# Optimization experiments

Hardware: AMD Instinct MI355X
Metric: run time of the kernel (lower is better)

Reference implementation:

```python
import jax, jax.numpy as jnp
import numpy as np

NUM_GRAPHS = 32
NODES_PER_GRAPH = 256
N = NUM_GRAPHS * NODES_PER_GRAPH
IN_CH, HID, OUT_CH = 64, 256, 32
K = 20
SPACE, PROP = 3, 2
NEG_SLOPE = 0.01  # F.leaky_relu default
BIG = 1e9         # cross-graph distance mask


def _glorot(key, shape):
    fan_in, fan_out = shape
    lim = (6.0 / (fan_in + fan_out)) ** 0.5
    return jax.random.uniform(key, shape, jnp.float32, -lim, lim)


def setup_inputs() -> dict:
    key = jax.random.key(0)
    ks = jax.random.split(key, 16)
    inp = {
        "x": jax.random.normal(ks[0], (N, IN_CH), jnp.float32),
        "batch": jnp.repeat(jnp.arange(NUM_GRAPHS, dtype=jnp.int32), NODES_PER_GRAPH),
    }
    dims = [(IN_CH, HID), (HID, HID), (HID, OUT_CH)]
    i = 1
    for li, (cin, cout) in enumerate(dims, start=1):
        inp[f"Ws{li}"] = _glorot(ks[i], (cin, SPACE)); i += 1
        inp[f"bs{li}"] = jnp.zeros((SPACE,), jnp.float32)
        inp[f"Wh{li}"] = _glorot(ks[i], (cin, PROP)); i += 1
        inp[f"bh{li}"] = jnp.zeros((PROP,), jnp.float32)
        inp[f"Wo{li}"] = _glorot(ks[i], (cin + PROP, cout)); i += 1
        inp[f"bo{li}"] = jnp.zeros((cout,), jnp.float32)
    return inp


def gravnet_conv(x, mask_add, Ws, bs, Wh, bh, Wo, bo):
    s = x @ Ws + bs                                     # [N,3] learned coords
    h = x @ Wh + bh                                     # [N,2] propagate feats
    s2 = jnp.sum(s * s, axis=1)
    d2 = s2[:, None] + s2[None, :] - 2.0 * (s @ s.T)    # [N,N] squared dists
    d2 = jnp.maximum(d2, 0.0) + mask_add                # block within-graph only
    neg_d2, idx = jax.lax.top_k(-d2, K)                 # kNN (includes self)
    w = jnp.exp(10.0 * neg_d2)                          # exp(-10 * d^2)
    agg = jnp.einsum('nk,nkp->np', w, h[idx])           # aggr='add'
    return jnp.concatenate([agg, x], axis=-1) @ Wo + bo  # lin(cat([out, x]))


def _leaky(h):
    return jnp.where(h >= 0, h, NEG_SLOPE * h)


def reference(x, batch,
              Ws1, bs1, Wh1, bh1, Wo1, bo1,
              Ws2, bs2, Wh2, bh2, Wo2, bo2,
              Ws3, bs3, Wh3, bh3, Wo3, bo3):
    mask_add = jnp.where(batch[:, None] == batch[None, :], 0.0, BIG).astype(x.dtype)
    # dropout p=0.0 -> identity
    h = _leaky(gravnet_conv(x, mask_add, Ws1, bs1, Wh1, bh1, Wo1, bo1))
    h = _leaky(gravnet_conv(h, mask_add, Ws2, bs2, Wh2, bh2, Wo2, bo2))
    out = gravnet_conv(h, mask_add, Ws3, bs3, Wh3, bh3, Wo3, bo3)
    # get_zero_nodes: first node of each contiguous graph segment
    b = jnp.concatenate([jnp.zeros((1,), batch.dtype), batch])
    diff = (b[1:] - b[:-1]).at[0].set(1)
    first_idx = jnp.nonzero(diff != 0, size=NUM_GRAPHS)[0]
    return out[first_idx]
```

## Files before the change

kernel.cpp:

```cpp
#include <hip/hip_runtime.h>
#include <hip/hip_bf16.h>


#define NGRAPH 32
#define GN 256
#define NTOT (NGRAPH*GN)
#define KNN 20
#define CTS 129

typedef __attribute__((ext_vector_type(8))) short bf16x8;
typedef __attribute__((ext_vector_type(4))) float f32x4;

__device__ __forceinline__ ushort f2bf(float x) {
    union { float f; unsigned u; } a; a.f = x;
    unsigned r = a.u + 0x7FFFu + ((a.u >> 16) & 1u);
    return (ushort)(r >> 16);
}
__device__ __forceinline__ float bf2f(ushort h) {
    union { unsigned u; float f; } b; b.u = ((unsigned)h) << 16;
    return b.f;
}
__device__ __forceinline__ bf16x8 ld8(const ushort* p) {
    return *reinterpret_cast<const bf16x8*>(p);
}
__device__ __forceinline__ unsigned pack2(ushort a, ushort b) {
    return (unsigned)a | ((unsigned)b << 16);
}

__global__ __launch_bounds__(256) void k_front(
    const float* __restrict__ X,
    const float* __restrict__ Ws1, const float* __restrict__ bs1,
    const float* __restrict__ Wh1, const float* __restrict__ bh1,
    const float* __restrict__ Wo1, const float* __restrict__ Wo2,
    const float* __restrict__ bs2, const float* __restrict__ bh2,
    const float* __restrict__ bs3, const float* __restrict__ bh3,
    ushort* __restrict__ Wt1hi, ushort* __restrict__ Wt1lo,
    ushort* __restrict__ Wt2hi, ushort* __restrict__ Wt2lo,
    ushort* __restrict__ Xhi, ushort* __restrict__ Xlo,
    float* __restrict__ s1, float* __restrict__ h1p,
    float* __restrict__ s2, float* __restrict__ h2p,
    float* __restrict__ s3, float* __restrict__ h3p)
{
    int b = blockIdx.x, tid = threadIdx.x;
    if (b < 2048) {
        int gw = b * 4 + (tid >> 6);
        int lane = tid & 63;
        float xv = X[(size_t)gw * 64 + lane];
        float a0 = xv * Ws1[lane * 3 + 0];
        float a1 = xv * Ws1[lane * 3 + 1];
        float a2 = xv * Ws1[lane * 3 + 2];
        float a3 = xv * Wh1[lane * 2 + 0];
        float a4 = xv * Wh1[lane * 2 + 1];
#pragma unroll
        for (int m = 1; m < 64; m <<= 1) {
            a0 += __shfl_xor(a0, m); a1 += __shfl_xor(a1, m); a2 += __shfl_xor(a2, m);
            a3 += __shfl_xor(a3, m); a4 += __shfl_xor(a4, m);
        }
        if (lane == 0) {
            s1[gw * 3 + 0] = a0 + bs1[0];
            s1[gw * 3 + 1] = a1 + bs1[1];
            s1[gw * 3 + 2] = a2 + bs1[2];
            h1p[gw * 2 + 0] = a3 + bh1[0];
            h1p[gw * 2 + 1] = a4 + bh1[1];
        }
    } else if (b < 2368) {
        int t = (b - 2048) * 256 + tid;
        if (t < 65536) {
            int n = t >> 8, c = t & 255;
            float v = Wo2[(size_t)(2 + c) * 256 + n];
            ushort hi = f2bf(v);
            Wt2hi[n * 256 + c] = hi;
            Wt2lo[n * 256 + c] = f2bf(v - bf2f(hi));
        } else {
            int u = t - 65536;
            int n = u >> 6, c = u & 63;
            float v = Wo1[(size_t)(2 + c) * 256 + n];
            ushort hi = f2bf(v);
            Wt1hi[n * 64 + c] = hi;
            Wt1lo[n * 64 + c] = f2bf(v - bf2f(hi));
        }
    } else if (b < 2688) {
        int u = (b - 2368) * 256 + tid;
        if (u < 24576)      s2[u] = bs2[u % 3];
        else if (u < 40960) { int w = u - 24576; h2p[w] = bh2[w & 1]; }
        else if (u < 65536) { int w = u - 40960; s3[w] = bs3[w % 3]; }
        else                { int w = u - 65536; h3p[w] = bh3[w & 1]; }
    } else {
        int t = (b - 2688) * 256 + tid;
        float2 v = *reinterpret_cast<const float2*>(&X[(size_t)t * 2]);
        ushort hx = f2bf(v.x), hy = f2bf(v.y);
        Xhi[t * 2 + 0] = hx; Xlo[t * 2 + 0] = f2bf(v.x - bf2f(hx));
        Xhi[t * 2 + 1] = hy; Xlo[t * 2 + 1] = f2bf(v.y - bf2f(hy));
    }
}

__device__ __forceinline__ void knn_row_agg(
    const float* __restrict__ s, const float* __restrict__ h,
    int base, int row, int lane, float& out0, float& out1)
{
    float s0 = s[row * 3 + 0], s1 = s[row * 3 + 1], s2 = s[row * 3 + 2];
    float s2row = s0 * s0 + s1 * s1 + s2 * s2;
    auto calc = [&](int j) {
        const float* sj = s + (size_t)(base + j) * 3;
        float t0 = sj[0], t1 = sj[1], t2 = sj[2];
        float s2j = t0 * t0 + t1 * t1 + t2 * t2;
        float dot = s0 * t0 + s1 * t1 + s2 * t2;
        float d2 = s2row + s2j - 2.0f * dot;
        return __float_as_uint(d2 > 0.f ? d2 : 0.f);
    };
    unsigned ua = calc(lane),       ub = calc(lane + 64);
    unsigned uc = calc(lane + 128), ud = calc(lane + 192);
    float2 hA = *reinterpret_cast<const float2*>(&h[(size_t)(base + lane) * 2]);
    float2 hB = *reinterpret_cast<const float2*>(&h[(size_t)(base + lane + 64) * 2]);
    float2 hC = *reinterpret_cast<const float2*>(&h[(size_t)(base + lane + 128) * 2]);
    float2 hD = *reinterpret_cast<const float2*>(&h[(size_t)(base + lane + 192) * 2]);

    float acc0 = 0.f, acc1 = 0.f;
#pragma unroll 1
    for (int it = 0; it < KNN; ++it) {
        unsigned bv = ua; float bh0 = hA.x, bh1 = hA.y;
        if (ub < bv) { bv = ub; bh0 = hB.x; bh1 = hB.y; }
        if (uc < bv) { bv = uc; bh0 = hC.x; bh1 = hC.y; }
        if (ud < bv) { bv = ud; bh0 = hD.x; bh1 = hD.y; }
        unsigned gv = bv;
#pragma unroll
        for (int m = 1; m < 64; m <<= 1) {
            unsigned o = __shfl_xor(gv, m);
            gv = o < gv ? o : gv;
        }
        float d2 = __uint_as_float(gv);
        if (d2 > 2.0f) break;
        unsigned long long mask = __ballot(bv == gv);
        int wl = __ffsll(mask) - 1;
        if (lane == wl) {
            float w = __expf(-10.0f * d2);
            acc0 = fmaf(w, bh0, acc0);
            acc1 = fmaf(w, bh1, acc1);
            ua = (ua == gv) ? 0xFFFFFFFFu : ua;
            ub = (ub == gv) ? 0xFFFFFFFFu : ub;
            uc = (uc == gv) ? 0xFFFFFFFFu : uc;
            ud = (ud == gv) ? 0xFFFFFFFFu : ud;
        }
    }
#pragma unroll
    for (int m = 1; m < 64; m <<= 1) {
        acc0 += __shfl_xor(acc0, m);
        acc1 += __shfl_xor(acc1, m);
    }
    out0 = acc0; out1 = acc1;
}

__global__ __launch_bounds__(256) void knn_kernel(
    const float* __restrict__ s, const float* __restrict__ h,
    float* __restrict__ agg)
{
    int gw = (int)(blockIdx.x * 4 + (threadIdx.x >> 6));
    int lane = threadIdx.x & 63;
    float a0, a1;
    knn_row_agg(s, h, gw & ~(GN - 1), gw, lane, a0, a1);
    if (lane == 0) {
        agg[gw * 2 + 0] = a0;
        agg[gw * 2 + 1] = a1;
    }
}

template<int K, int CMODE>
__global__ __launch_bounds__(512) void gemm_fused(
    const ushort* __restrict__ Ahi, const ushort* __restrict__ Alo,
    const ushort* __restrict__ Bhi, const ushort* __restrict__ Blo,
    const float* __restrict__ Wfull, const float* __restrict__ bias,
    const float* __restrict__ agg,
    float* __restrict__ Cf, ushort* __restrict__ Chi, ushort* __restrict__ Clo,
    const float* __restrict__ Wsn, const float* __restrict__ Whn,
    float* __restrict__ s_out, float* __restrict__ h_out)
{
    __shared__ float CT[64 * CTS];
    __shared__ float part[64 * 8 * 5];

    const int tid = threadIdx.x;
    const int lane = tid & 63, wid = tid >> 6;
    const int wm = wid >> 2, wn = wid & 3;
    const int m0 = blockIdx.x * 64, n0 = blockIdx.y * 128;

    f32x4 acc[2][2];
#pragma unroll
    for (int mi = 0; mi < 2; ++mi)
#pragma unroll
        for (int ni = 0; ni < 2; ++ni)
            acc[mi][ni] = (f32x4){0.f, 0.f, 0.f, 0.f};

#pragma unroll 2
    for (int kof = 0; kof < K; kof += 32) {
        int kch = kof + (lane >> 4) * 8;
        bf16x8 ah[2], al[2], bh[2], bl[2];
#pragma unroll
        for (int mi = 0; mi < 2; ++mi) {
            size_t off = (size_t)(m0 + wm * 32 + mi * 16 + (lane & 15)) * K + kch;
            ah[mi] = ld8(Ahi + off); al[mi] = ld8(Alo + off);
        }
#pragma unroll
        for (int ni = 0; ni < 2; ++ni) {
            size_t off = (size_t)(n0 + wn * 32 + ni * 16 + (lane & 15)) * K + kch;
            bh[ni] = ld8(Bhi + off); bl[ni] = ld8(Blo + off);
        }
#pragma unroll
        for (int mi = 0; mi < 2; ++mi)
#pragma unroll
            for (int ni = 0; ni < 2; ++ni) {
                acc[mi][ni] = __builtin_amdgcn_mfma_f32_16x16x32_bf16(ah[mi], bh[ni], acc[mi][ni], 0, 0, 0);
                acc[mi][ni] = __builtin_amdgcn_mfma_f32_16x16x32_bf16(ah[mi], bl[ni], acc[mi][ni], 0, 0, 0);
                acc[mi][ni] = __builtin_amdgcn_mfma_f32_16x16x32_bf16(al[mi], bh[ni], acc[mi][ni], 0, 0, 0);
            }
    }

#pragma unroll
    for (int ni = 0; ni < 2; ++ni) {
        int nl = wn * 32 + ni * 16 + (lane & 15);
        int n = n0 + nl;
        float w0 = Wfull[n], w1 = Wfull[256 + n], bz = bias[n];
#pragma unroll
        for (int mi = 0; mi < 2; ++mi) {
            int mb = wm * 32 + mi * 16 + ((lane >> 4) << 2);
#pragma unroll
            for (int r = 0; r < 4; ++r) {
                int ml = mb + r, m = m0 + ml;
                float v = acc[mi][ni][r] + fmaf(agg[m * 2 + 0], w0, fmaf(agg[m * 2 + 1], w1, bz));
                v = v >= 0.f ? v : 0.01f * v;
                CT[ml * CTS + nl] = v;
                if (CMODE == 1 && (m & 255) == 0) Cf[(m >> 8) * 256 + n] = v;
            }
        }
    }
    __syncthreads();

    if (CMODE == 0) {
        int row = tid >> 3, cbase = (tid & 7) * 16;
        size_t m = (size_t)(m0 + row);
#pragma unroll
        for (int j = 0; j < 2; ++j) {
            int c = cbase + j * 8;
            ushort hi[8], lo[8];
#pragma unroll
            for (int t = 0; t < 8; ++t) {
                float v = CT[row * CTS + c + t];
                hi[t] = f2bf(v);
                lo[t] = f2bf(v - bf2f(hi[t]));
            }
            uint4 wh = make_uint4(pack2(hi[0], hi[1]), pack2(hi[2], hi[3]),
                                  pack2(hi[4], hi[5]), pack2(hi[6], hi[7]));
            uint4 wl = make_uint4(pack2(lo[0], lo[1]), pack2(lo[2], lo[3]),
                                  pack2(lo[4], lo[5]), pack2(lo[6], lo[7]));
            *reinterpret_cast<uint4*>(&Chi[m * 256 + n0 + c]) = wh;
            *reinterpret_cast<uint4*>(&Clo[m * 256 + n0 + c]) = wl;
        }
    }

    {
        int row = tid & 63, sub = tid >> 6;
        float p0 = 0.f, p1 = 0.f, p2 = 0.f, p3 = 0.f, p4 = 0.f;
#pragma unroll
        for (int i = 0; i < 16; ++i) {
            int c = sub * 16 + i;
            float v = CT[row * CTS + c];
            int n = n0 + c;
            p0 = fmaf(v, Wsn[n * 3 + 0], p0);
            p1 = fmaf(v, Wsn[n * 3 + 1], p1);
            p2 = fmaf(v, Wsn[n * 3 + 2], p2);
            p3 = fmaf(v, Whn[n * 2 + 0], p3);
            p4 = fmaf(v, Whn[n * 2 + 1], p4);
        }
        float* pp = &part[(row * 8 + sub) * 5];
        pp[0] = p0; pp[1] = p1; pp[2] = p2; pp[3] = p3; pp[4] = p4;
    }
    __syncthreads();
    if (tid < 320) {
        int row = tid / 5, o = tid - row * 5;
        float sum = 0.f;
#pragma unroll
        for (int k = 0; k < 8; ++k) sum += part[(row * 8 + k) * 5 + o];
        if (o < 3) atomicAdd(&s_out[(m0 + row) * 3 + o], sum);
        else       atomicAdd(&h_out[(m0 + row) * 2 + (o - 3)], sum);
    }
}

__global__ __launch_bounds__(256) void knn3_final(
    const float* __restrict__ s, const float* __restrict__ h,
    const float* __restrict__ h2c,
    const float* __restrict__ Wo, const float* __restrict__ bo,
    float* __restrict__ out)
{
    __shared__ float aggL[2];
    __shared__ float pm[8][32];
    int g = blockIdx.x, tid = threadIdx.x;
    if (tid < 64) {
        float a0, a1;
        knn_row_agg(s, h, g * GN, g * GN, tid, a0, a1);
        if (tid == 0) { aggL[0] = a0; aggL[1] = a1; }
    }
    __syncthreads();
    int o = tid & 31, seg = tid >> 5;
    const float* xr = h2c + g * 256;
    float p = 0.f;
#pragma unroll
    for (int i = 0; i < 32; ++i) {
        int c = seg * 32 + i;
        p = fmaf(xr[c], Wo[(2 + c) * 32 + o], p);
    }
    pm[seg][o] = p;
    __syncthreads();
    if (tid < 32) {
        float acc = fmaf(aggL[0], Wo[o], fmaf(aggL[1], Wo[32 + o], bo[o]));
#pragma unroll
        for (int k = 0; k < 8; ++k) acc += pm[k][o];
        out[g * 32 + o] = acc;
    }
}

extern "C" void kernel_launch(void* const* d_in, const int* in_sizes, int n_in,
                              void* d_out, int out_size, void* d_ws, size_t ws_size,
                              hipStream_t stream) {
    const float* X   = (const float*)d_in[0];
    const float* Ws1 = (const float*)d_in[2];  const float* bs1 = (const float*)d_in[3];
    const float* Wh1 = (const float*)d_in[4];  const float* bh1 = (const float*)d_in[5];
    const float* Wo1 = (const float*)d_in[6];  const float* bo1 = (const float*)d_in[7];
    const float* Ws2 = (const float*)d_in[8];  const float* bs2 = (const float*)d_in[9];
    const float* Wh2 = (const float*)d_in[10]; const float* bh2 = (const float*)d_in[11];
    const float* Wo2 = (const float*)d_in[12]; const float* bo2 = (const float*)d_in[13];
    const float* Ws3 = (const float*)d_in[14]; const float* bs3 = (const float*)d_in[15];
    const float* Wh3 = (const float*)d_in[16]; const float* bh3 = (const float*)d_in[17];
    const float* Wo3 = (const float*)d_in[18]; const float* bo3 = (const float*)d_in[19];

    float* p = (float*)d_ws;
    float* s1   = p; p += NTOT * 3;
    float* hp1  = p; p += NTOT * 2;
    float* s2   = p; p += NTOT * 3;
    float* hp2  = p; p += NTOT * 2;
    float* s3   = p; p += NTOT * 3;
    float* hp3  = p; p += NTOT * 2;
    float* aggb = p; p += NTOT * 2;
    float* h2c  = p; p += 32 * 256;
    ushort* q = (ushort*)p;
    ushort* Xhi  = q; q += (size_t)NTOT * 64;
    ushort* Xlo  = q; q += (size_t)NTOT * 64;
    ushort* h1hi = q; q += (size_t)NTOT * 256;
    ushort* h1lo = q; q += (size_t)NTOT * 256;
    ushort* Wt1hi = q; q += 256 * 64;
    ushort* Wt1lo = q; q += 256 * 64;
    ushort* Wt2hi = q; q += 256 * 256;
    ushort* Wt2lo = q; q += 256 * 256;

    k_front<<<3712, 256, 0, stream>>>(X, Ws1, bs1, Wh1, bh1, Wo1, Wo2,
                                      bs2, bh2, bs3, bh3,
                                      Wt1hi, Wt1lo, Wt2hi, Wt2lo, Xhi, Xlo,
                                      s1, hp1, s2, hp2, s3, hp3);
    knn_kernel<<<2048, 256, 0, stream>>>(s1, hp1, aggb);
    gemm_fused<64, 0><<<dim3(128, 2), 512, 0, stream>>>(Xhi, Xlo, Wt1hi, Wt1lo,
                                                        Wo1, bo1, aggb,
                                                        nullptr, h1hi, h1lo,
                                                        Ws2, Wh2, s2, hp2);
    knn_kernel<<<2048, 256, 0, stream>>>(s2, hp2, aggb);
    gemm_fused<256, 1><<<dim3(128, 2), 512, 0, stream>>>(h1hi, h1lo, Wt2hi, Wt2lo,
                                                         Wo2, bo2, aggb,
                                                         h2c, nullptr, nullptr,
                                                         Ws3, Wh3, s3, hp3);
    knn3_final<<<NGRAPH, 256, 0, stream>>>(s3, hp3, h2c, Wo3, bo3, (float*)d_out);
}
```

Baseline: 79.99 us.

## Fuse layer-1 projection and kNN into front kernel; use DPP wave reductions

The layer-1 coordinate/propagate projection and the first kNN aggregation now run inside the front kernel. Each block recomputes its graph's 256 projections into shared memory and handles 16 rows, which removes one launch and the s1/h1 round trip through global memory. The wave-wide min and sum reductions switch from shuffle butterflies to DPP row operations plus readlane, and the winning lane now picks its neighbour with a single branch chain. The cost is that the projection is recomputed 16 times per graph, and mixing kNN blocks with conversion blocks in one grid may cause uneven load.

```diff
diff --git a/kernel.cpp b/kernel.cpp
--- a/kernel.cpp
+++ b/kernel.cpp
@@ -27,7 +27,63 @@
     return (unsigned)a | ((unsigned)b << 16);
 }
 
-__global__ __launch_bounds__(256) void k_front(
+#define DPP_MIN(v, ctrl, rmask) { \
+    unsigned _t = (unsigned)__builtin_amdgcn_update_dpp((int)(v), (int)(v), ctrl, rmask, 0xf, false); \
+    (v) = _t < (v) ? _t : (v); }
+__device__ __forceinline__ unsigned wave_min_u32(unsigned v) {
+    DPP_MIN(v, 0x111, 0xf)
+    DPP_MIN(v, 0x112, 0xf)
+    DPP_MIN(v, 0x114, 0xf)
+    DPP_MIN(v, 0x118, 0xf)
+    DPP_MIN(v, 0x142, 0xa)
+    DPP_MIN(v, 0x143, 0xc)
+    return (unsigned)__builtin_amdgcn_readlane((int)v, 63);
+}
+#define DPP_ADD(v, ctrl, rmask) { \
+    float _t = __int_as_float(__builtin_amdgcn_update_dpp(0, __float_as_int(v), ctrl, rmask, 0xf, true)); \
+    (v) += _t; }
+__device__ __forceinline__ float wave_sum_f32(float v) {
+    DPP_ADD(v, 0x111, 0xf)
+    DPP_ADD(v, 0x112, 0xf)
+    DPP_ADD(v, 0x114, 0xf)
+    DPP_ADD(v, 0x118, 0xf)
+    DPP_ADD(v, 0x142, 0xa)
+    DPP_ADD(v, 0x143, 0xc)
+    return __int_as_float(__builtin_amdgcn_readlane(__float_as_int(v), 63));
+}
+
+__device__ __forceinline__ void knn_extract(
+    unsigned ua, unsigned ub, unsigned uc, unsigned ud,
+    float2 hA, float2 hB, float2 hC, float2 hD,
+    int lane, float& out0, float& out1)
+{
+    float acc0 = 0.f, acc1 = 0.f;
+#pragma unroll 1
+    for (int it = 0; it < KNN; ++it) {
+        unsigned m1 = ua < ub ? ua : ub;
+        unsigned m2 = uc < ud ? uc : ud;
+        unsigned bv = m1 < m2 ? m1 : m2;
+        unsigned gv = wave_min_u32(bv);
+        float d2 = __uint_as_float(gv);
+        if (d2 > 2.0f) break;
+        float w = __expf(-10.0f * d2);
+        unsigned long long mask = __ballot(bv == gv);
+        int wl = __ffsll(mask) - 1;
+        if (lane == wl) {
+            float h0, h1;
+            if (ua == gv)      { h0 = hA.x; h1 = hA.y; ua = 0xFFFFFFFFu; }
+            else if (ub == gv) { h0 = hB.x; h1 = hB.y; ub = 0xFFFFFFFFu; }
+            else if (uc == gv) { h0 = hC.x; h1 = hC.y; uc = 0xFFFFFFFFu; }
+            else               { h0 = hD.x; h1 = hD.y; ud = 0xFFFFFFFFu; }
+            acc0 = fmaf(w, h0, acc0);
+            acc1 = fmaf(w, h1, acc1);
+        }
+    }
+    out0 = wave_sum_f32(acc0);
+    out1 = wave_sum_f32(acc1);
+}
+
+__global__ __launch_bounds__(256) void knn1_mega(
     const float* __restrict__ X,
     const float* __restrict__ Ws1, const float* __restrict__ bs1,
     const float* __restrict__ Wh1, const float* __restrict__ bh1,
@@ -37,34 +93,72 @@
     ushort* __restrict__ Wt1hi, ushort* __restrict__ Wt1lo,
     ushort* __restrict__ Wt2hi, ushort* __restrict__ Wt2lo,
     ushort* __restrict__ Xhi, ushort* __restrict__ Xlo,
-    float* __restrict__ s1, float* __restrict__ h1p,
     float* __restrict__ s2, float* __restrict__ h2p,
-    float* __restrict__ s3, float* __restrict__ h3p)
+    float* __restrict__ s3, float* __restrict__ h3p,
+    float* __restrict__ agg)
 {
+    __shared__ float sh5[256 * 5];
     int b = blockIdx.x, tid = threadIdx.x;
-    if (b < 2048) {
-        int gw = b * 4 + (tid >> 6);
-        int lane = tid & 63;
-        float xv = X[(size_t)gw * 64 + lane];
-        float a0 = xv * Ws1[lane * 3 + 0];
-        float a1 = xv * Ws1[lane * 3 + 1];
-        float a2 = xv * Ws1[lane * 3 + 2];
-        float a3 = xv * Wh1[lane * 2 + 0];
-        float a4 = xv * Wh1[lane * 2 + 1];
-#pragma unroll
-        for (int m = 1; m < 64; m <<= 1) {
-            a0 += __shfl_xor(a0, m); a1 += __shfl_xor(a1, m); a2 += __shfl_xor(a2, m);
-            a3 += __shfl_xor(a3, m); a4 += __shfl_xor(a4, m);
-        }
-        if (lane == 0) {
-            s1[gw * 3 + 0] = a0 + bs1[0];
-            s1[gw * 3 + 1] = a1 + bs1[1];
-            s1[gw * 3 + 2] = a2 + bs1[2];
-            h1p[gw * 2 + 0] = a3 + bh1[0];
-            h1p[gw * 2 + 1] = a4 + bh1[1];
-        }
-    } else if (b < 2368) {
-        int t = (b - 2048) * 256 + tid;
+    if (b < 512) {
+        int g = b >> 4;
+        const float* Xg = X + (size_t)g * (GN * 64);
+        {
+            float a0 = 0.f, a1 = 0.f, a2 = 0.f, a3 = 0.f, a4 = 0.f;
+            const float* xr = Xg + tid * 64;
+#pragma unroll 4
+            for (int c0 = 0; c0 < 64; c0 += 4) {
+                float4 v = *reinterpret_cast<const float4*>(&xr[c0]);
+                float xv[4] = {v.x, v.y, v.z, v.w};
+#pragma unroll
+                for (int j = 0; j < 4; ++j) {
+                    int c = c0 + j;
+                    a0 = fmaf(xv[j], Ws1[c * 3 + 0], a0);
+                    a1 = fmaf(xv[j], Ws1[c * 3 + 1], a1);
+                    a2 = fmaf(xv[j], Ws1[c * 3 + 2], a2);
+                    a3 = fmaf(xv[j], Wh1[c * 2 + 0], a3);
+                    a4 = fmaf(xv[j], Wh1[c * 2 + 1], a4);
+                }
+            }
+            sh5[tid * 5 + 0] = a0 + bs1[0];
+            sh5[tid * 5 + 1] = a1 + bs1[1];
+            sh5[tid * 5 + 2] = a2 + bs1[2];
+            sh5[tid * 5 + 3] = a3 + bh1[0];
+            sh5[tid * 5 + 4] = a4 + bh1[1];
+        }
+        __syncthreads();
+        int lane = tid & 63, wid = tid >> 6;
+        float sjx[4], sjy[4], sjz[4], s2j[4];
+        float2 hs[4];
+#pragma unroll
+        for (int t = 0; t < 4; ++t) {
+            int j = lane + 64 * t;
+            float x = sh5[j * 5 + 0], y = sh5[j * 5 + 1], z = sh5[j * 5 + 2];
+            sjx[t] = x; sjy[t] = y; sjz[t] = z;
+            s2j[t] = x * x + y * y + z * z;
+            hs[t] = make_float2(sh5[j * 5 + 3], sh5[j * 5 + 4]);
+        }
+        int rbase = (b & 15) * 16 + wid * 4;
+#pragma unroll 1
+        for (int rr = 0; rr < 4; ++rr) {
+            int rl = rbase + rr;
+            float s0 = sh5[rl * 5 + 0], s1v = sh5[rl * 5 + 1], s2v = sh5[rl * 5 + 2];
+            float s2row = s0 * s0 + s1v * s1v + s2v * s2v;
+            unsigned key[4];
+#pragma unroll
+            for (int t = 0; t < 4; ++t) {
+                float dot = s0 * sjx[t] + s1v * sjy[t] + s2v * sjz[t];
+                float d2 = s2row + s2j[t] - 2.0f * dot;
+                key[t] = __float_as_uint(d2 > 0.f ? d2 : 0.f);
+            }
+            float a0, a1;
+            knn_extract(key[0], key[1], key[2], key[3], hs[0], hs[1], hs[2], hs[3], lane, a0, a1);
+            if (lane == 0) {
+                agg[(g * GN + rl) * 2 + 0] = a0;
+                agg[(g * GN + rl) * 2 + 1] = a1;
+            }
+        }
+    } else if (b < 832) {
+        int t = (b - 512) * 256 + tid;
         if (t < 65536) {
             int n = t >> 8, c = t & 255;
             float v = Wo2[(size_t)(2 + c) * 256 + n];
@@ -79,75 +173,19 @@
             Wt1hi[n * 64 + c] = hi;
             Wt1lo[n * 64 + c] = f2bf(v - bf2f(hi));
         }
-    } else if (b < 2688) {
-        int u = (b - 2368) * 256 + tid;
+    } else if (b < 1152) {
+        int u = (b - 832) * 256 + tid;
         if (u < 24576)      s2[u] = bs2[u % 3];
         else if (u < 40960) { int w = u - 24576; h2p[w] = bh2[w & 1]; }
         else if (u < 65536) { int w = u - 40960; s3[w] = bs3[w % 3]; }
         else                { int w = u - 65536; h3p[w] = bh3[w & 1]; }
     } else {
-        int t = (b - 2688) * 256 + tid;
+        int t = (b - 1152) * 256 + tid;
         float2 v = *reinterpret_cast<const float2*>(&X[(size_t)t * 2]);
         ushort hx = f2bf(v.x), hy = f2bf(v.y);
         Xhi[t * 2 + 0] = hx; Xlo[t * 2 + 0] = f2bf(v.x - bf2f(hx));
         Xhi[t * 2 + 1] = hy; Xlo[t * 2 + 1] = f2bf(v.y - bf2f(hy));
     }
-}
-
-__device__ __forceinline__ void knn_row_agg(
-    const float* __restrict__ s, const float* __restrict__ h,
-    int base, int row, int lane, float& out0, float& out1)
-{
-    float s0 = s[row * 3 + 0], s1 = s[row * 3 + 1], s2 = s[row * 3 + 2];
-    float s2row = s0 * s0 + s1 * s1 + s2 * s2;
-    auto calc = [&](int j) {
-        const float* sj = s + (size_t)(base + j) * 3;
-        float t0 = sj[0], t1 = sj[1], t2 = sj[2];
-        float s2j = t0 * t0 + t1 * t1 + t2 * t2;
-        float dot = s0 * t0 + s1 * t1 + s2 * t2;
-        float d2 = s2row + s2j - 2.0f * dot;
-        return __float_as_uint(d2 > 0.f ? d2 : 0.f);
-    };
-    unsigned ua = calc(lane),       ub = calc(lane + 64);
-    unsigned uc = calc(lane + 128), ud = calc(lane + 192);
-    float2 hA = *reinterpret_cast<const float2*>(&h[(size_t)(base + lane) * 2]);
-    float2 hB = *reinterpret_cast<const float2*>(&h[(size_t)(base + lane + 64) * 2]);
-    float2 hC = *reinterpret_cast<const float2*>(&h[(size_t)(base + lane + 128) * 2]);
-    float2 hD = *reinterpret_cast<const float2*>(&h[(size_t)(base + lane + 192) * 2]);
-
-    float acc0 = 0.f, acc1 = 0.f;
-#pragma unroll 1
-    for (int it = 0; it < KNN; ++it) {
-        unsigned bv = ua; float bh0 = hA.x, bh1 = hA.y;
-        if (ub < bv) { bv = ub; bh0 = hB.x; bh1 = hB.y; }
-        if (uc < bv) { bv = uc; bh0 = hC.x; bh1 = hC.y; }
-        if (ud < bv) { bv = ud; bh0 = hD.x; bh1 = hD.y; }
-        unsigned gv = bv;
-#pragma unroll
-        for (int m = 1; m < 64; m <<= 1) {
-            unsigned o = __shfl_xor(gv, m);
-            gv = o < gv ? o : gv;
-        }
-        float d2 = __uint_as_float(gv);
-        if (d2 > 2.0f) break;
-        unsigned long long mask = __ballot(bv == gv);
-        int wl = __ffsll(mask) - 1;
-        if (lane == wl) {
-            float w = __expf(-10.0f * d2);
-            acc0 = fmaf(w, bh0, acc0);
-            acc1 = fmaf(w, bh1, acc1);
-            ua = (ua == gv) ? 0xFFFFFFFFu : ua;
-            ub = (ub == gv) ? 0xFFFFFFFFu : ub;
-            uc = (uc == gv) ? 0xFFFFFFFFu : uc;
-            ud = (ud == gv) ? 0xFFFFFFFFu : ud;
-        }
-    }
-#pragma unroll
-    for (int m = 1; m < 64; m <<= 1) {
-        acc0 += __shfl_xor(acc0, m);
-        acc1 += __shfl_xor(acc1, m);
-    }
-    out0 = acc0; out1 = acc1;
 }
 
 __global__ __launch_bounds__(256) void knn_kernel(
@@ -156,8 +194,21 @@
 {
     int gw = (int)(blockIdx.x * 4 + (threadIdx.x >> 6));
     int lane = threadIdx.x & 63;
+    int base = gw & ~(GN - 1);
+    float s0 = s[gw * 3 + 0], s1v = s[gw * 3 + 1], s2v = s[gw * 3 + 2];
+    float s2row = s0 * s0 + s1v * s1v + s2v * s2v;
+    unsigned key[4]; float2 hs[4];
+#pragma unroll
+    for (int t = 0; t < 4; ++t) {
+        int j = base + lane + 64 * t;
+        float x = s[j * 3 + 0], y = s[j * 3 + 1], z = s[j * 3 + 2];
+        float dot = s0 * x + s1v * y + s2v * z;
+        float d2 = s2row + (x * x + y * y + z * z) - 2.0f * dot;
+        key[t] = __float_as_uint(d2 > 0.f ? d2 : 0.f);
+        hs[t] = *reinterpret_cast<const float2*>(&h[(size_t)j * 2]);
+    }
     float a0, a1;
-    knn_row_agg(s, h, gw & ~(GN - 1), gw, lane, a0, a1);
+    knn_extract(key[0], key[1], key[2], key[3], hs[0], hs[1], hs[2], hs[3], lane, a0, a1);
     if (lane == 0) {
         agg[gw * 2 + 0] = a0;
         agg[gw * 2 + 1] = a1;
@@ -293,9 +344,23 @@
     __shared__ float pm[8][32];
     int g = blockIdx.x, tid = threadIdx.x;
     if (tid < 64) {
+        int lane = tid;
+        int base = g * GN, row = g * GN;
+        float s0 = s[row * 3 + 0], s1v = s[row * 3 + 1], s2v = s[row * 3 + 2];
+        float s2row = s0 * s0 + s1v * s1v + s2v * s2v;
+        unsigned key[4]; float2 hs[4];
+#pragma unroll
+        for (int t = 0; t < 4; ++t) {
+            int j = base + lane + 64 * t;
+            float x = s[j * 3 + 0], y = s[j * 3 + 1], z = s[j * 3 + 2];
+            float dot = s0 * x + s1v * y + s2v * z;
+            float d2 = s2row + (x * x + y * y + z * z) - 2.0f * dot;
+            key[t] = __float_as_uint(d2 > 0.f ? d2 : 0.f);
+            hs[t] = *reinterpret_cast<const float2*>(&h[(size_t)j * 2]);
+        }
         float a0, a1;
-        knn_row_agg(s, h, g * GN, g * GN, tid, a0, a1);
-        if (tid == 0) { aggL[0] = a0; aggL[1] = a1; }
+        knn_extract(key[0], key[1], key[2], key[3], hs[0], hs[1], hs[2], hs[3], lane, a0, a1);
+        if (lane == 0) { aggL[0] = a0; aggL[1] = a1; }
     }
     __syncthreads();
     int o = tid & 31, seg = tid >> 5;
@@ -331,8 +396,6 @@
     const float* Wo3 = (const float*)d_in[18]; const float* bo3 = (const float*)d_in[19];
 
     float* p = (float*)d_ws;
-    float* s1   = p; p += NTOT * 3;
-    float* hp1  = p; p += NTOT * 2;
     float* s2   = p; p += NTOT * 3;
     float* hp2  = p; p += NTOT * 2;
     float* s3   = p; p += NTOT * 3;
@@ -349,11 +412,10 @@
     ushort* Wt2hi = q; q += 256 * 256;
     ushort* Wt2lo = q; q += 256 * 256;
 
-    k_front<<<3712, 256, 0, stream>>>(X, Ws1, bs1, Wh1, bh1, Wo1, Wo2,
-                                      bs2, bh2, bs3, bh3,
-                                      Wt1hi, Wt1lo, Wt2hi, Wt2lo, Xhi, Xlo,
-                                      s1, hp1, s2, hp2, s3, hp3);
-    knn_kernel<<<2048, 256, 0, stream>>>(s1, hp1, aggb);
+    knn1_mega<<<2176, 256, 0, stream>>>(X, Ws1, bs1, Wh1, bh1, Wo1, Wo2,
+                                        bs2, bh2, bs3, bh3,
+                                        Wt1hi, Wt1lo, Wt2hi, Wt2lo, Xhi, Xlo,
+                                        s2, hp2, s3, hp3, aggb);
     gemm_fused<64, 0><<<dim3(128, 2), 512, 0, stream>>>(Xhi, Xlo, Wt1hi, Wt1lo,
                                                         Wo1, bo1, aggb,
                                                         nullptr, h1hi, h1lo,
```

Measured after the change: 78.77 us. No clear change (-1.5%).
